# Kernel optimization log

Hardware: AMD Instinct MI355X
Metric: run time of the kernel (lower is better)

Reference implementation:

```python
import jax, jax.numpy as jnp
import numpy as np


def gru_cell(inp, h, wi, wh, bi, bh):
    # torch nn.GRU cell math: gates ordered (r, z, n)
    gi = inp @ wi.T + bi          # [3H]
    gh = h @ wh.T + bh            # [3H]
    ir, iz, inn = jnp.split(gi, 3, axis=-1)
    hr, hz, hn = jnp.split(gh, 3, axis=-1)
    r = jax.nn.sigmoid(ir + hr)
    z = jax.nn.sigmoid(iz + hz)
    n = jnp.tanh(inn + r * hn)
    return (1.0 - z) * n + z * h


def setup_inputs() -> dict:
    key = jax.random.key(0)
    C, L = 1024, 2048  # input_size / hidden_size, sequence length
    ks = jax.random.split(key, 11)
    x = jax.random.normal(ks[0], (1, L, C), jnp.float32)
    # attention: Linear(2C, 1), weight ~ N(0, 0.01), bias = -1 (per module init)
    attn_w = jax.random.normal(ks[1], (1, 2 * C), jnp.float32) * 0.01
    attn_b = jnp.full((1,), -1.0, jnp.float32)
    # GRU default torch init: U(-1/sqrt(H), 1/sqrt(H))
    s = 1.0 / np.sqrt(C).astype(np.float32)
    u = lambda k, shape: jax.random.uniform(k, shape, jnp.float32, -s, s)
    w_ih0 = u(ks[2], (3 * C, C)); w_hh0 = u(ks[3], (3 * C, C))
    b_ih0 = u(ks[4], (3 * C,));   b_hh0 = u(ks[5], (3 * C,))
    w_ih1 = u(ks[6], (3 * C, C)); w_hh1 = u(ks[7], (3 * C, C))
    b_ih1 = u(ks[8], (3 * C,));   b_hh1 = u(ks[9], (3 * C,))
    return {"x": x, "attn_w": attn_w, "attn_b": attn_b,
            "w_ih0": w_ih0, "w_hh0": w_hh0, "b_ih0": b_ih0, "b_hh0": b_hh0,
            "w_ih1": w_ih1, "w_hh1": w_hh1, "b_ih1": b_ih1, "b_hh1": b_hh1,
            "lengths": L}


def reference(x, attn_w, attn_b, w_ih0, w_hh0, b_ih0, b_hh0,
              w_ih1, w_hh1, b_ih1, b_hh1, lengths):
    x0 = x[0]                     # [L, C]; batch must be 1
    L, C = x0.shape
    dt = x.dtype

    def step(carry, _):
        out, h0, h1 = carry       # out: [C], h0/h1: [C]
        # attention: score each timestep against previous output
        concated = jnp.concatenate(
            [jnp.broadcast_to(out, (L, C)), x0], axis=1)  # [L, 2C]
        logits = concated @ attn_w.T + attn_b             # [L, 1]
        a = jax.nn.softmax(logits, axis=0)                # softmax over L
        av = jnp.sum(a * x0, axis=0)                      # [C] context vector
        # 2-layer GRU, one timestep
        h0n = gru_cell(av, h0, w_ih0, w_hh0, b_ih0, b_hh0)
        h1n = gru_cell(h0n, h1, w_ih1, w_hh1, b_ih1, b_hh1)
        return (h1n, h0n, h1n), h1n

    init = (jnp.zeros((C,), dt), jnp.zeros((C,), dt), jnp.zeros((C,), dt))
    (_, h0, h1), outs = jax.lax.scan(step, init, None, length=lengths)
    outputs = outs[None]                                  # [1, L, C]
    previous_state = jnp.stack([h0, h1])[:, None, :]      # [2, 1, C]
    return outputs, previous_state
```

## Files before the change

kernel.cpp:

```cpp
#include <hip/hip_runtime.h>
#include <math.h>

#define CC 1024
#define LL 2048
#define NWG 256
#define NT 256

typedef float f4 __attribute__((ext_vector_type(4)));
typedef unsigned u4 __attribute__((ext_vector_type(4)));

#define PKT_PAR 4096
#define PKT_ARR 1024
#define WS_FLAGS 8192
#define WS_REL 16384
#define WS_LOGITS 16448
#define WS_AV (WS_LOGITS + LL)
#define WS_MEMSET_BYTES ((WS_REL + 64) * 4)

__device__ __forceinline__ float aload(const float* p) {
  return __hip_atomic_load(p, __ATOMIC_RELAXED, __HIP_MEMORY_SCOPE_AGENT);
}
__device__ __forceinline__ void astore(float* p, float v) {
  __hip_atomic_store(p, v, __ATOMIC_RELAXED, __HIP_MEMORY_SCOPE_AGENT);
}
__device__ __forceinline__ float sigm(float x) { return 1.0f / (1.0f + __expf(-x)); }
__device__ __forceinline__ float tanh_(float x) { return 2.0f / (1.0f + __expf(-2.0f * x)) - 1.0f; }

__device__ __forceinline__ float dot4(f4 a, f4 b) {
  return fmaf(a.x, b.x, fmaf(a.y, b.y, fmaf(a.z, b.z, a.w * b.w)));
}

__device__ __forceinline__ void ld16u_x4(const unsigned* p0, const unsigned* p1,
                                         const unsigned* p2, const unsigned* p3,
                                         u4& a, u4& b, u4& c, u4& d) {
  asm volatile(
      "global_load_dwordx4 %0, %4, off sc0 sc1\n\t"
      "global_load_dwordx4 %1, %5, off sc0 sc1\n\t"
      "global_load_dwordx4 %2, %6, off sc0 sc1\n\t"
      "global_load_dwordx4 %3, %7, off sc0 sc1\n\t"
      "s_waitcnt vmcnt(0)"
      : "=v"(a), "=v"(b), "=v"(c), "=v"(d)
      : "v"(p0), "v"(p1), "v"(p2), "v"(p3)
      : "memory");
}
__device__ __forceinline__ void st16u(unsigned* p, u4 v) {
  asm volatile("global_store_dwordx4 %0, %1, off sc0 sc1" ::"v"(p), "v"(v) : "memory");
}

__device__ __forceinline__ void gbar(unsigned* ws_u, unsigned epoch) {
  __syncthreads();
  if (blockIdx.x == 0) {
    const int i = threadIdx.x;
    if (i > 0 && i < NWG) {
      unsigned* slot = ws_u + WS_FLAGS + i * 32;
      while (__hip_atomic_load(slot, __ATOMIC_RELAXED, __HIP_MEMORY_SCOPE_AGENT) < epoch) {
      }
      (void)__hip_atomic_load(slot, __ATOMIC_ACQUIRE, __HIP_MEMORY_SCOPE_AGENT);
    }
    __syncthreads();
    if (i == 0)
      __hip_atomic_store(ws_u + WS_REL, epoch, __ATOMIC_RELEASE, __HIP_MEMORY_SCOPE_AGENT);
    __syncthreads();
  } else {
    if (threadIdx.x == 0) {
      __hip_atomic_store(ws_u + WS_FLAGS + blockIdx.x * 32, epoch, __ATOMIC_RELEASE,
                         __HIP_MEMORY_SCOPE_AGENT);
      unsigned* rel = ws_u + WS_REL;
      while (__hip_atomic_load(rel, __ATOMIC_RELAXED, __HIP_MEMORY_SCOPE_AGENT) < epoch) {
      }
      (void)__hip_atomic_load(rel, __ATOMIC_ACQUIRE, __HIP_MEMORY_SCOPE_AGENT);
    }
    __syncthreads();
  }
}

#define PIN9(b)                                                                       \
  asm volatile("" : "+v"(W[b + 0]), "+v"(W[b + 1]), "+v"(W[b + 2]), "+v"(W[b + 3]),   \
                    "+v"(W[b + 4]), "+v"(W[b + 5]), "+v"(W[b + 6]), "+v"(W[b + 7]),   \
                    "+v"(W[b + 8]))

__global__ __launch_bounds__(NT, 1) void decoder_kernel(
    const float* __restrict__ x, const float* __restrict__ attn_w,
    const float* __restrict__ w_ih0, const float* __restrict__ w_hh0,
    const float* __restrict__ b_ih0, const float* __restrict__ b_hh0,
    const float* __restrict__ w_ih1, const float* __restrict__ w_hh1,
    const float* __restrict__ b_ih1, const float* __restrict__ b_hh1,
    float* __restrict__ out, float* __restrict__ ws) {
  const int g = blockIdx.x;
  const int tid = threadIdx.x;
  const int lane = tid & 63;
  const int w = tid >> 6;

  unsigned* ws_u = (unsigned*)ws;

  __shared__ __align__(16) float h0s[CC];
  __shared__ __align__(16) float h1s[CC];
  __shared__ float cgi0[12], cbh0[12], cbh1[12], cbi1[12];
  __shared__ float red[NT];

  {
    const float* w2 = attn_w + CC;
#pragma unroll
    for (int s = 0; s < 2; ++s) {
      int t = 8 * g + 2 * w + s;
      const float* xr = x + (size_t)t * CC;
      float p = 0.f;
#pragma unroll
      for (int k = 0; k < 4; ++k) {
        f4 xa = *(const f4*)(xr + 256 * k + 4 * lane);
        f4 wa = *(const f4*)(w2 + 256 * k + 4 * lane);
        p += dot4(xa, wa);
      }
#pragma unroll
      for (int off = 32; off; off >>= 1) p += __shfl_xor(p, off, 64);
      if (lane == 0) astore(ws + WS_LOGITS + t, p);
    }
  }
  gbar(ws_u, 1);

  {
    float myl[8];
#pragma unroll
    for (int s = 0; s < 8; ++s) myl[s] = aload(ws + WS_LOGITS + tid + 256 * s);
    float lm = myl[0];
#pragma unroll
    for (int s = 1; s < 8; ++s) lm = fmaxf(lm, myl[s]);
    red[tid] = lm;
    __syncthreads();
    for (int stp = 128; stp; stp >>= 1) {
      if (tid < stp) red[tid] = fmaxf(red[tid], red[tid + stp]);
      __syncthreads();
    }
    float m = red[0];
    __syncthreads();
    float myw[8];
    float ls = 0.f;
#pragma unroll
    for (int s = 0; s < 8; ++s) {
      myw[s] = __expf(myl[s] - m);
      ls += myw[s];
    }
    red[tid] = ls;
    __syncthreads();
    for (int stp = 128; stp; stp >>= 1) {
      if (tid < stp) red[tid] += red[tid + stp];
      __syncthreads();
    }
    float invZ = 1.0f / red[0];
    __syncthreads();
    float acc[4] = {0.f, 0.f, 0.f, 0.f};
#pragma unroll
    for (int s = 0; s < 8; ++s) {
      int t = tid + 256 * s;
      f4 xa = *(const f4*)(x + (size_t)t * CC + 4 * g);
      acc[0] = fmaf(myw[s], xa.x, acc[0]);
      acc[1] = fmaf(myw[s], xa.y, acc[1]);
      acc[2] = fmaf(myw[s], xa.z, acc[2]);
      acc[3] = fmaf(myw[s], xa.w, acc[3]);
    }
    for (int i = 0; i < 4; ++i) {
      red[tid] = acc[i];
      __syncthreads();
      for (int stp = 128; stp; stp >>= 1) {
        if (tid < stp) red[tid] += red[tid + stp];
        __syncthreads();
      }
      if (tid == 0) astore(ws + WS_AV + 4 * g + i, red[0] * invZ);
      __syncthreads();
    }
  }
  gbar(ws_u, 2);

#pragma unroll
  for (int i = 0; i < 4; ++i) h0s[4 * tid + i] = aload(ws + WS_AV + 4 * tid + i);
  __syncthreads();
  {
    f4 hc[4];
#pragma unroll
    for (int k = 0; k < 4; ++k) hc[k] = *(const f4*)&h0s[256 * k + 4 * lane];
#pragma unroll
    for (int jj = 0; jj < 3; ++jj) {
      int j = 3 * w + jj;
      int gate = j >> 2, e = j & 3;
      int row = gate * CC + 4 * g + e;
      const float* wr = w_ih0 + (size_t)row * CC;
      float p = 0.f;
#pragma unroll
      for (int k = 0; k < 4; ++k) p += dot4(*(const f4*)(wr + 256 * k + 4 * lane), hc[k]);
#pragma unroll
      for (int off = 32; off; off >>= 1) p += __shfl_xor(p, off, 64);
      if (lane == 0) cgi0[j] = p + b_ih0[row];
    }
  }
  if (tid < 12) {
    int gate = tid >> 2, e = tid & 3;
    int row = gate * CC + 4 * g + e;
    cbh0[tid] = b_hh0[row];
    cbh1[tid] = b_hh1[row];
    cbi1[tid] = b_ih1[row];
  }

  f4 W[36];
#pragma unroll
  for (int G = 0; G < 3; ++G) {
    size_t row = (size_t)(G * CC + 4 * g + w) << 10;
#pragma unroll
    for (int k = 0; k < 4; ++k) {
      W[(0 * 3 + G) * 4 + k] = *(const f4*)(w_hh0 + row + 256 * k + 4 * lane);
      W[(1 * 3 + G) * 4 + k] = *(const f4*)(w_hh1 + row + 256 * k + 4 * lane);
      W[(2 * 3 + G) * 4 + k] = *(const f4*)(w_ih1 + row + 256 * k + 4 * lane);
    }
  }
#pragma unroll
  for (int i = 0; i < 4; ++i) {
    h0s[4 * tid + i] = 0.f;
    h1s[4 * tid + i] = 0.f;
  }
  __syncthreads();

  float h0last = 0.f;
  unsigned* pkt0 = ws_u;
  unsigned* pkt1 = ws_u + PKT_PAR;

  for (int tau = 0; tau <= LL; ++tau) {
    PIN9(0);
    PIN9(9);
    PIN9(18);
    PIN9(27);
    if (tau > 0) {
      const unsigned ut = (unsigned)tau;
      unsigned* base = (tau & 1) ? pkt1 : pkt0;
      const unsigned* pA = base + 0 * PKT_ARR + 4 * tid;
      const unsigned* pB = base + 1 * PKT_ARR + 4 * tid;
      const unsigned* pC = base + 2 * PKT_ARR + 4 * tid;
      const unsigned* pD = base + 3 * PKT_ARR + 4 * tid;
      u4 a, b, c, d;
      do {
        ld16u_x4(pA, pB, pC, pD, a, b, c, d);
      } while (a.w != ut || b.w != ut || c.w != ut || d.w != ut);
      f4 v0, v1;
      v0.x = __uint_as_float(a.x);
      v0.y = __uint_as_float(b.x);
      v0.z = __uint_as_float(c.x);
      v0.w = __uint_as_float(d.x);
      v1.x = __uint_as_float(a.y);
      v1.y = __uint_as_float(b.y);
      v1.z = __uint_as_float(c.y);
      v1.w = __uint_as_float(d.y);
      *(f4*)&h0s[4 * tid] = v0;
      *(f4*)&h1s[4 * tid] = v1;
    }
    __syncthreads();
    f4 hc0[4], hc1[4];
#pragma unroll
    for (int k = 0; k < 4; ++k) {
      hc0[k] = *(const f4*)&h0s[256 * k + 4 * lane];
      hc1[k] = *(const f4*)&h1s[256 * k + 4 * lane];
    }
    float h0prev = h0s[4 * g + w];
    float h1prev = h1s[4 * g + w];
    float p[9];
#pragma unroll
    for (int G = 0; G < 3; ++G) {
      float pa = 0.f, pb = 0.f, pc = 0.f;
#pragma unroll
      for (int k = 0; k < 4; ++k) {
        pa += dot4(W[(0 * 3 + G) * 4 + k], hc0[k]);
        pb += dot4(W[(1 * 3 + G) * 4 + k], hc1[k]);
        pc += dot4(W[(2 * 3 + G) * 4 + k], hc0[k]);
      }
      p[G] = pa;
      p[3 + G] = pb;
      p[6 + G] = pc;
    }
#pragma unroll
    for (int off = 32; off; off >>= 1) {
#pragma unroll
      for (int i = 0; i < 9; ++i) p[i] += __shfl_xor(p[i], off, 64);
    }
    float r0 = sigm(cgi0[w] + p[0] + cbh0[w]);
    float z0 = sigm(cgi0[4 + w] + p[1] + cbh0[4 + w]);
    float n0 = tanh_(cgi0[8 + w] + r0 * (p[2] + cbh0[8 + w]));
    float h0new = (1.f - z0) * n0 + z0 * h0prev;

    float r1 = sigm(p[6] + cbi1[w] + p[3] + cbh1[w]);
    float z1 = sigm(p[7] + cbi1[4 + w] + p[4] + cbh1[4 + w]);
    float n1 = tanh_(p[8] + cbi1[8 + w] + r1 * (p[5] + cbh1[8 + w]));
    float h1new = (1.f - z1) * n1 + z1 * h1prev;

    if (lane == 0) {
      if (tau < LL) {
        u4 pk;
        pk.x = __float_as_uint(h0new);
        pk.y = __float_as_uint((tau > 0) ? h1new : 0.f);
        pk.z = 0u;
        pk.w = (unsigned)(tau + 1);
        unsigned* dst = (((tau + 1) & 1) ? pkt1 : pkt0) + w * PKT_ARR + 4 * g;
        st16u(dst, pk);
      }
      if (tau > 0) out[(size_t)(tau - 1) * CC + 4 * g + w] = h1new;
      if (tau == LL) {
        out[(size_t)LL * CC + 4 * g + w] = h0last;
        out[(size_t)LL * CC + CC + 4 * g + w] = h1new;
      }
    }
    if (tau == LL - 1) h0last = h0new;
    __syncthreads();
  }
}

extern "C" void kernel_launch(void* const* d_in, const int* in_sizes, int n_in,
                              void* d_out, int out_size, void* d_ws, size_t ws_size,
                              hipStream_t stream) {
  const float* x = (const float*)d_in[0];
  const float* attn_w = (const float*)d_in[1];
  const float* w_ih0 = (const float*)d_in[3];
  const float* w_hh0 = (const float*)d_in[4];
  const float* b_ih0 = (const float*)d_in[5];
  const float* b_hh0 = (const float*)d_in[6];
  const float* w_ih1 = (const float*)d_in[7];
  const float* w_hh1 = (const float*)d_in[8];
  const float* b_ih1 = (const float*)d_in[9];
  const float* b_hh1 = (const float*)d_in[10];
  float* out = (float*)d_out;
  float* ws = (float*)d_ws;

  hipMemsetAsync(d_ws, 0, WS_MEMSET_BYTES, stream);

  void* args[] = {&x,     &attn_w, &w_ih0, &w_hh0, &b_ih0, &b_hh0,
                  &w_ih1, &w_hh1,  &b_ih1, &b_hh1, &out,   &ws};
  hipLaunchCooperativeKernel((void*)decoder_kernel, dim3(NWG), dim3(NT), args, 0,
                             stream);
}
```

Before: 7.813 ms.

## Move recurrent weights to LDS and issue packet loads early before barrier

```diff
diff --git a/kernel.cpp b/kernel.cpp
--- a/kernel.cpp
+++ b/kernel.cpp
@@ -30,19 +30,12 @@
   return fmaf(a.x, b.x, fmaf(a.y, b.y, fmaf(a.z, b.z, a.w * b.w)));
 }
 
-__device__ __forceinline__ void ld16u_x4(const unsigned* p0, const unsigned* p1,
-                                         const unsigned* p2, const unsigned* p3,
-                                         u4& a, u4& b, u4& c, u4& d) {
-  asm volatile(
-      "global_load_dwordx4 %0, %4, off sc0 sc1\n\t"
-      "global_load_dwordx4 %1, %5, off sc0 sc1\n\t"
-      "global_load_dwordx4 %2, %6, off sc0 sc1\n\t"
-      "global_load_dwordx4 %3, %7, off sc0 sc1\n\t"
-      "s_waitcnt vmcnt(0)"
-      : "=v"(a), "=v"(b), "=v"(c), "=v"(d)
-      : "v"(p0), "v"(p1), "v"(p2), "v"(p3)
-      : "memory");
-}
+__device__ __forceinline__ u4 ld16v(const unsigned* p) {
+  u4 r;
+  asm volatile("global_load_dwordx4 %0, %1, off sc0 sc1" : "=v"(r) : "v"(p) : "memory");
+  return r;
+}
+__device__ __forceinline__ void vm0() { asm volatile("s_waitcnt vmcnt(0)" ::: "memory"); }
 __device__ __forceinline__ void st16u(unsigned* p, u4 v) {
   asm volatile("global_store_dwordx4 %0, %1, off sc0 sc1" ::"v"(p), "v"(v) : "memory");
 }
@@ -73,11 +66,6 @@
     __syncthreads();
   }
 }
-
-#define PIN9(b)                                                                       \
-  asm volatile("" : "+v"(W[b + 0]), "+v"(W[b + 1]), "+v"(W[b + 2]), "+v"(W[b + 3]),   \
-                    "+v"(W[b + 4]), "+v"(W[b + 5]), "+v"(W[b + 6]), "+v"(W[b + 7]),   \
-                    "+v"(W[b + 8]))
 
 __global__ __launch_bounds__(NT, 1) void decoder_kernel(
     const float* __restrict__ x, const float* __restrict__ attn_w,
@@ -90,9 +78,11 @@
   const int tid = threadIdx.x;
   const int lane = tid & 63;
   const int w = tid >> 6;
+  const int eg = 4 * g + w;
 
   unsigned* ws_u = (unsigned*)ws;
 
+  extern __shared__ float wlds[];
   __shared__ __align__(16) float h0s[CC];
   __shared__ __align__(16) float h1s[CC];
   __shared__ float cgi0[12], cbh0[12], cbh1[12], cbi1[12];
@@ -200,16 +190,12 @@
     cbi1[tid] = b_ih1[row];
   }
 
-  f4 W[36];
-#pragma unroll
-  for (int G = 0; G < 3; ++G) {
-    size_t row = (size_t)(G * CC + 4 * g + w) << 10;
-#pragma unroll
-    for (int k = 0; k < 4; ++k) {
-      W[(0 * 3 + G) * 4 + k] = *(const f4*)(w_hh0 + row + 256 * k + 4 * lane);
-      W[(1 * 3 + G) * 4 + k] = *(const f4*)(w_hh1 + row + 256 * k + 4 * lane);
-      W[(2 * 3 + G) * 4 + k] = *(const f4*)(w_ih1 + row + 256 * k + 4 * lane);
-    }
+#pragma unroll
+  for (int j = 0; j < 36; ++j) {
+    int ww = j / 9, r = j % 9, mat = r / 3, G = r % 3;
+    const float* src = (mat == 0 ? w_hh0 : (mat == 1 ? w_hh1 : w_ih1)) +
+                       ((size_t)(G * CC + 4 * g + ww) << 10);
+    *(f4*)&wlds[j * 1024 + 4 * tid] = *(const f4*)(src + 4 * tid);
   }
 #pragma unroll
   for (int i = 0; i < 4; ++i) {
@@ -221,12 +207,10 @@
   float h0last = 0.f;
   unsigned* pkt0 = ws_u;
   unsigned* pkt1 = ws_u + PKT_PAR;
+  u4 qa, qb, qc, qd;
+  const float* wr9 = wlds + (w * 9) * 1024;
 
   for (int tau = 0; tau <= LL; ++tau) {
-    PIN9(0);
-    PIN9(9);
-    PIN9(18);
-    PIN9(27);
     if (tau > 0) {
       const unsigned ut = (unsigned)tau;
       unsigned* base = (tau & 1) ? pkt1 : pkt0;
@@ -234,19 +218,23 @@
       const unsigned* pB = base + 1 * PKT_ARR + 4 * tid;
       const unsigned* pC = base + 2 * PKT_ARR + 4 * tid;
       const unsigned* pD = base + 3 * PKT_ARR + 4 * tid;
-      u4 a, b, c, d;
-      do {
-        ld16u_x4(pA, pB, pC, pD, a, b, c, d);
-      } while (a.w != ut || b.w != ut || c.w != ut || d.w != ut);
+      vm0();
+      while (qa.w != ut || qb.w != ut || qc.w != ut || qd.w != ut) {
+        qa = ld16v(pA);
+        qb = ld16v(pB);
+        qc = ld16v(pC);
+        qd = ld16v(pD);
+        vm0();
+      }
       f4 v0, v1;
-      v0.x = __uint_as_float(a.x);
-      v0.y = __uint_as_float(b.x);
-      v0.z = __uint_as_float(c.x);
-      v0.w = __uint_as_float(d.x);
-      v1.x = __uint_as_float(a.y);
-      v1.y = __uint_as_float(b.y);
-      v1.z = __uint_as_float(c.y);
-      v1.w = __uint_as_float(d.y);
+      v0.x = __uint_as_float(qa.x);
+      v0.y = __uint_as_float(qb.x);
+      v0.z = __uint_as_float(qc.x);
+      v0.w = __uint_as_float(qd.x);
+      v1.x = __uint_as_float(qa.y);
+      v1.y = __uint_as_float(qb.y);
+      v1.z = __uint_as_float(qc.y);
+      v1.w = __uint_as_float(qd.y);
       *(f4*)&h0s[4 * tid] = v0;
       *(f4*)&h1s[4 * tid] = v1;
     }
@@ -257,17 +245,18 @@
       hc0[k] = *(const f4*)&h0s[256 * k + 4 * lane];
       hc1[k] = *(const f4*)&h1s[256 * k + 4 * lane];
     }
-    float h0prev = h0s[4 * g + w];
-    float h1prev = h1s[4 * g + w];
+    float h0prev = h0s[eg];
+    float h1prev = h1s[eg];
     float p[9];
 #pragma unroll
     for (int G = 0; G < 3; ++G) {
       float pa = 0.f, pb = 0.f, pc = 0.f;
 #pragma unroll
       for (int k = 0; k < 4; ++k) {
-        pa += dot4(W[(0 * 3 + G) * 4 + k], hc0[k]);
-        pb += dot4(W[(1 * 3 + G) * 4 + k], hc1[k]);
-        pc += dot4(W[(2 * 3 + G) * 4 + k], hc0[k]);
+        int off = 256 * k + 4 * lane;
+        pa += dot4(*(const f4*)&wr9[(0 * 3 + G) * 1024 + off], hc0[k]);
+        pb += dot4(*(const f4*)&wr9[(1 * 3 + G) * 1024 + off], hc1[k]);
+        pc += dot4(*(const f4*)&wr9[(2 * 3 + G) * 1024 + off], hc0[k]);
       }
       p[G] = pa;
       p[3 + G] = pb;
@@ -298,13 +287,20 @@
         unsigned* dst = (((tau + 1) & 1) ? pkt1 : pkt0) + w * PKT_ARR + 4 * g;
         st16u(dst, pk);
       }
-      if (tau > 0) out[(size_t)(tau - 1) * CC + 4 * g + w] = h1new;
+      if (tau > 0) out[(size_t)(tau - 1) * CC + eg] = h1new;
       if (tau == LL) {
-        out[(size_t)LL * CC + 4 * g + w] = h0last;
-        out[(size_t)LL * CC + CC + 4 * g + w] = h1new;
+        out[(size_t)LL * CC + eg] = h0last;
+        out[(size_t)LL * CC + CC + eg] = h1new;
       }
     }
     if (tau == LL - 1) h0last = h0new;
+    if (tau < LL) {
+      unsigned* nb = ((tau + 1) & 1) ? pkt1 : pkt0;
+      qa = ld16v(nb + 0 * PKT_ARR + 4 * tid);
+      qb = ld16v(nb + 1 * PKT_ARR + 4 * tid);
+      qc = ld16v(nb + 2 * PKT_ARR + 4 * tid);
+      qd = ld16v(nb + 3 * PKT_ARR + 4 * tid);
+    }
     __syncthreads();
   }
 }
@@ -325,10 +321,17 @@
   float* out = (float*)d_out;
   float* ws = (float*)d_ws;
 
+  static int attr_set = 0;
+  if (!attr_set) {
+    hipFuncSetAttribute((const void*)decoder_kernel,
+                        hipFuncAttributeMaxDynamicSharedMemorySize, 36 * 1024 * 4);
+    attr_set = 1;
+  }
+
   hipMemsetAsync(d_ws, 0, WS_MEMSET_BYTES, stream);
 
   void* args[] = {&x,     &attn_w, &w_ih0, &w_hh0, &b_ih0, &b_hh0,
                   &w_ih1, &w_hh1,  &b_ih1, &b_hh1, &out,   &ws};
-  hipLaunchCooperativeKernel((void*)decoder_kernel, dim3(NWG), dim3(NT), args, 0,
-                             stream);
-}
+  hipLaunchCooperativeKernel((void*)decoder_kernel, dim3(NWG), dim3(NT), args,
+                             36 * 1024 * 4, stream);
+}
```

Result: slower. 8.512 ms (+8.9%).
